# Optimization experiments

Measured on AMD Instinct MI355X. Metric: run time of the kernel, lower is better.

## Reference

```python
import jax, jax.numpy as jnp
import numpy as np

N_USERS = 100000
N_GAMES = 50000
D = 128
E = 1600000


def setup_inputs() -> dict:
    key = jax.random.key(0)
    k1, k2, k3, k4 = jax.random.split(key, 4)
    user_h = jax.random.normal(k1, (N_USERS, D), dtype=jnp.float32)
    game_h = jax.random.normal(k2, (N_GAMES, D), dtype=jnp.float32)
    src_idx = jax.random.randint(k3, (E,), 0, N_USERS, dtype=jnp.int64)
    dst_idx = jax.random.randint(k4, (E,), 0, N_GAMES, dtype=jnp.int64)
    return {"user_h": user_h, "game_h": game_h, "src_idx": src_idx, "dst_idx": dst_idx}


def reference(user_h, game_h, src_idx, dst_idx):
    # DGL fn.u_dot_v: gather src/dst node features along the edge list,
    # then per-edge dot product. Output shape [E, 1] (DGL keeps last dim).
    u = user_h[src_idx]          # [E, D] gather
    v = game_h[dst_idx]          # [E, D] gather
    score = jnp.sum(u * v, axis=-1, keepdims=True)  # [E, 1]
    return score
```

## Files before the change

### kernel.cpp

```cpp
#include <hip/hip_runtime.h>


#define DIM 128
#define NB 64
#define CAP 28160
#define BPB 782
#define N_USERS_C 100000u
#define EPB_A 4096

__global__ void init_cursors(unsigned* __restrict__ cur) {
    int i = threadIdx.x;
    if (i < NB) cur[i * 32] = (unsigned)(i * CAP);
}

__device__ inline unsigned bf16rn(float f) {
    unsigned x = __float_as_uint(f);
    return (x + 0x7FFFu + ((x >> 16) & 1u)) >> 16;
}

__global__ void __launch_bounds__(256) prep_fused(
    const float* __restrict__ user_h, const float* __restrict__ game_h,
    const int* __restrict__ src_idx, const int* __restrict__ dst_idx, int E,
    unsigned* __restrict__ cursors, uint2* __restrict__ records,
    uint4* __restrict__ user_bf, uint4* __restrict__ game_bf,
    int nscat, int nublk, int nu8, int ng8)
{
    __shared__ unsigned hist[NB];
    __shared__ unsigned base_s[NB];
    __shared__ unsigned lcur[NB];
    int bid = blockIdx.x;
    int tid = threadIdx.x;

    if (bid >= nscat) {
        const float* in;
        uint4* outp;
        int i, n8;
        if (bid < nscat + nublk) {
            i = (bid - nscat) * 256 + tid;  n8 = nu8;  in = user_h;  outp = user_bf;
        } else {
            i = (bid - nscat - nublk) * 256 + tid;  n8 = ng8;  in = game_h;  outp = game_bf;
        }
        if (i < n8) {
            const float4* in4 = (const float4*)in;
            float4 a = in4[2 * i];
            float4 b = in4[2 * i + 1];
            uint4 o;
            o.x = bf16rn(a.x) | (bf16rn(a.y) << 16);
            o.y = bf16rn(a.z) | (bf16rn(a.w) << 16);
            o.z = bf16rn(b.x) | (bf16rn(b.y) << 16);
            o.w = bf16rn(b.z) | (bf16rn(b.w) << 16);
            outp[i] = o;
        }
        return;
    }

    long long start = (long long)bid * EPB_A;

    if (tid < NB) hist[tid] = 0u;
    __syncthreads();

    for (int k = 0; k < EPB_A / 256; ++k) {
        long long e = start + k * 256 + tid;
        if (e < E) {
            unsigned s = (unsigned)src_idx[e];
            unsigned b = (s * (unsigned)NB) / N_USERS_C;
            atomicAdd(&hist[b], 1u);
        }
    }
    __syncthreads();

    if (tid < NB) {
        base_s[tid] = atomicAdd(&cursors[tid * 32], hist[tid]);
        lcur[tid] = 0u;
    }
    __syncthreads();

    for (int k = 0; k < EPB_A / 256; ++k) {
        long long e = start + k * 256 + tid;
        if (e < E) {
            unsigned s = (unsigned)src_idx[e];
            unsigned d = (unsigned)dst_idx[e];
            unsigned b = (s * (unsigned)NB) / N_USERS_C;
            unsigned r = atomicAdd(&lcur[b], 1u);
            unsigned pos = base_s[b] + r;
            if (pos < (unsigned)((b + 1) * CAP)) {
                uint2 rec;
                rec.x = s | ((d & 0x7FFFu) << 17);
                rec.y = (d >> 15) | ((unsigned)e << 1);
                records[pos] = rec;
            }
        }
    }
}

__device__ inline float dot8_bf16(uint4 a, uint4 b) {
    float s;
    s  = __uint_as_float(a.x << 16)          * __uint_as_float(b.x << 16);
    s += __uint_as_float(a.x & 0xFFFF0000u)  * __uint_as_float(b.x & 0xFFFF0000u);
    s += __uint_as_float(a.y << 16)          * __uint_as_float(b.y << 16);
    s += __uint_as_float(a.y & 0xFFFF0000u)  * __uint_as_float(b.y & 0xFFFF0000u);
    s += __uint_as_float(a.z << 16)          * __uint_as_float(b.z << 16);
    s += __uint_as_float(a.z & 0xFFFF0000u)  * __uint_as_float(b.z & 0xFFFF0000u);
    s += __uint_as_float(a.w << 16)          * __uint_as_float(b.w << 16);
    s += __uint_as_float(a.w & 0xFFFF0000u)  * __uint_as_float(b.w & 0xFFFF0000u);
    return s;
}

__global__ void __launch_bounds__(256) edge_dot_bucketed_bf16(
    const uint4* __restrict__ user_bf, const uint4* __restrict__ game_bf,
    const unsigned* __restrict__ cursors, const uint2* __restrict__ records,
    float* __restrict__ out)
{
    int bid = blockIdx.x;
    int x = bid & 7;
    int n = bid >> 3;
    int bq = n / BPB;
    int chunk = n - bq * BPB;
    int b = x + 8 * bq;

    int count = (int)(cursors[b * 32] - (unsigned)(b * CAP));
    if (count > CAP) count = CAP;
    const uint2* __restrict__ rec = records + (size_t)b * CAP;

    int g    = threadIdx.x >> 4;
    int lane = threadIdx.x & 15;

    for (int j0 = chunk * 32; j0 < count; j0 += BPB * 32) {
        int j = j0 + 2 * g;
        if (j >= count) continue;
        bool has1 = (j + 1 < count);

        uint2 r0 = rec[j];
        uint2 r1 = has1 ? rec[j + 1] : r0;

        unsigned s0 = r0.x & 0x1FFFFu;
        unsigned d0 = ((r0.x >> 17) & 0x7FFFu) | ((r0.y & 1u) << 15);
        unsigned e0 = r0.y >> 1;
        unsigned s1 = r1.x & 0x1FFFFu;
        unsigned d1 = ((r1.x >> 17) & 0x7FFFu) | ((r1.y & 1u) << 15);
        unsigned e1 = r1.y >> 1;

        uint4 ua = user_bf[(size_t)s0 * 16 + lane];
        uint4 va = game_bf[(size_t)d0 * 16 + lane];
        uint4 ub = user_bf[(size_t)s1 * 16 + lane];
        uint4 vb = game_bf[(size_t)d1 * 16 + lane];

        float sum0 = dot8_bf16(ua, va);
        float sum1 = dot8_bf16(ub, vb);

        sum0 += __shfl_xor(sum0, 1);  sum1 += __shfl_xor(sum1, 1);
        sum0 += __shfl_xor(sum0, 2);  sum1 += __shfl_xor(sum1, 2);
        sum0 += __shfl_xor(sum0, 4);  sum1 += __shfl_xor(sum1, 4);
        sum0 += __shfl_xor(sum0, 8);  sum1 += __shfl_xor(sum1, 8);

        if (lane == 0) {
            out[e0] = sum0;
            if (has1) out[e1] = sum1;
        }
    }
}

__global__ void __launch_bounds__(256) edge_dot_kernel(
    const float* __restrict__ user_h,
    const float* __restrict__ game_h,
    const int* __restrict__ src_idx,
    const int* __restrict__ dst_idx,
    float* __restrict__ out,
    int E)
{
    int tid  = blockIdx.x * blockDim.x + threadIdx.x;
    int g    = tid >> 4;
    int lane = tid & 15;
    long long e0 = (long long)g * 2;
    if (e0 >= E) return;
    bool has1 = (e0 + 1 < E);

    int s0 = src_idx[e0];
    int d0 = dst_idx[e0];
    int s1 = has1 ? src_idx[e0 + 1] : s0;
    int d1 = has1 ? dst_idx[e0 + 1] : d0;

    const float4* __restrict__ u0 = (const float4*)(user_h + (size_t)s0 * DIM);
    const float4* __restrict__ v0 = (const float4*)(game_h + (size_t)d0 * DIM);
    const float4* __restrict__ u1 = (const float4*)(user_h + (size_t)s1 * DIM);
    const float4* __restrict__ v1 = (const float4*)(game_h + (size_t)d1 * DIM);

    float4 ua0 = u0[lane];
    float4 ua1 = u0[lane + 16];
    float4 va0 = v0[lane];
    float4 va1 = v0[lane + 16];
    float4 ub0 = u1[lane];
    float4 ub1 = u1[lane + 16];
    float4 vb0 = v1[lane];
    float4 vb1 = v1[lane + 16];

    float sum0 = ua0.x * va0.x + ua0.y * va0.y + ua0.z * va0.z + ua0.w * va0.w
               + ua1.x * va1.x + ua1.y * va1.y + ua1.z * va1.z + ua1.w * va1.w;
    float sum1 = ub0.x * vb0.x + ub0.y * vb0.y + ub0.z * vb0.z + ub0.w * vb0.w
               + ub1.x * vb1.x + ub1.y * vb1.y + ub1.z * vb1.z + ub1.w * vb1.w;

    sum0 += __shfl_xor(sum0, 1);  sum1 += __shfl_xor(sum1, 1);
    sum0 += __shfl_xor(sum0, 2);  sum1 += __shfl_xor(sum1, 2);
    sum0 += __shfl_xor(sum0, 4);  sum1 += __shfl_xor(sum1, 4);
    sum0 += __shfl_xor(sum0, 8);  sum1 += __shfl_xor(sum1, 8);

    if (lane == 0) {
        out[e0] = sum0;
        if (has1) out[e0 + 1] = sum1;
    }
}

extern "C" void kernel_launch(void* const* d_in, const int* in_sizes, int n_in,
                              void* d_out, int out_size, void* d_ws, size_t ws_size,
                              hipStream_t stream) {
    const float* user_h  = (const float*)d_in[0];
    const float* game_h  = (const float*)d_in[1];
    const int*   src_idx = (const int*)d_in[2];
    const int*   dst_idx = (const int*)d_in[3];
    float*       out     = (float*)d_out;

    int E       = in_sizes[2];
    int n_user  = in_sizes[0];
    int n_game  = in_sizes[1];

    size_t rec_bytes = (size_t)NB * CAP * sizeof(uint2);
    size_t ws_full   = 8192 + rec_bytes + (size_t)n_user * 2 + (size_t)n_game * 2;

    if (ws_size < ws_full || E > (1 << 21)) {
        long long nblocks = ((long long)E + 31) / 32;
        edge_dot_kernel<<<(int)nblocks, 256, 0, stream>>>(
            user_h, game_h, src_idx, dst_idx, out, E);
        return;
    }

    unsigned* cursors = (unsigned*)d_ws;
    uint2*    records = (uint2*)((char*)d_ws + 8192);
    uint4*    user_bf = (uint4*)((char*)d_ws + 8192 + rec_bytes);
    uint4*    game_bf = (uint4*)((char*)user_bf + (size_t)n_user * 2);

    init_cursors<<<1, 64, 0, stream>>>(cursors);

    int nu8 = n_user / 8, ng8 = n_game / 8;
    int nscat = (E + EPB_A - 1) / EPB_A;
    int nublk = (nu8 + 255) / 256;
    int ngblk = (ng8 + 255) / 256;

    prep_fused<<<nscat + nublk + ngblk, 256, 0, stream>>>(
        user_h, game_h, src_idx, dst_idx, E,
        cursors, records, user_bf, game_bf,
        nscat, nublk, nu8, ng8);

    edge_dot_bucketed_bf16<<<NB * BPB, 256, 0, stream>>>(
        user_bf, game_bf, cursors, records, out);
}
```

Measured before the change: 105.7 us.

## Read user features as fp32 directly, convert only game table to bf16

Drops the bf16 conversion of the user table. Because edges are bucketed by source, user rows are read in fp32 straight from the input while only the game table is converted to bf16. This removes a full user-table read and write pass in prep, at the cost of twice the bytes per user-row gather in the dot kernel. The change also replaces the cursor-init kernel with a memset, making cursors zero-based, and keeps the src/dst indices in registers so the scatter pass does not reload them.

```diff
diff --git a/kernel.cpp b/kernel.cpp
--- a/kernel.cpp
+++ b/kernel.cpp
@@ -8,22 +8,17 @@
 #define N_USERS_C 100000u
 #define EPB_A 4096
 
-__global__ void init_cursors(unsigned* __restrict__ cur) {
-    int i = threadIdx.x;
-    if (i < NB) cur[i * 32] = (unsigned)(i * CAP);
-}
-
 __device__ inline unsigned bf16rn(float f) {
     unsigned x = __float_as_uint(f);
     return (x + 0x7FFFu + ((x >> 16) & 1u)) >> 16;
 }
 
 __global__ void __launch_bounds__(256) prep_fused(
-    const float* __restrict__ user_h, const float* __restrict__ game_h,
+    const float* __restrict__ game_h,
     const int* __restrict__ src_idx, const int* __restrict__ dst_idx, int E,
     unsigned* __restrict__ cursors, uint2* __restrict__ records,
-    uint4* __restrict__ user_bf, uint4* __restrict__ game_bf,
-    int nscat, int nublk, int nu8, int ng8)
+    uint4* __restrict__ game_bf,
+    int nscat, int ng8)
 {
     __shared__ unsigned hist[NB];
     __shared__ unsigned base_s[NB];
@@ -32,16 +27,9 @@
     int tid = threadIdx.x;
 
     if (bid >= nscat) {
-        const float* in;
-        uint4* outp;
-        int i, n8;
-        if (bid < nscat + nublk) {
-            i = (bid - nscat) * 256 + tid;  n8 = nu8;  in = user_h;  outp = user_bf;
-        } else {
-            i = (bid - nscat - nublk) * 256 + tid;  n8 = ng8;  in = game_h;  outp = game_bf;
-        }
-        if (i < n8) {
-            const float4* in4 = (const float4*)in;
+        int i = (bid - nscat) * 256 + tid;
+        if (i < ng8) {
+            const float4* in4 = (const float4*)game_h;
             float4 a = in4[2 * i];
             float4 b = in4[2 * i + 1];
             uint4 o;
@@ -49,21 +37,29 @@
             o.y = bf16rn(a.z) | (bf16rn(a.w) << 16);
             o.z = bf16rn(b.x) | (bf16rn(b.y) << 16);
             o.w = bf16rn(b.z) | (bf16rn(b.w) << 16);
-            outp[i] = o;
+            game_bf[i] = o;
         }
         return;
     }
 
     long long start = (long long)bid * EPB_A;
+    unsigned ss[16], dd[16];
+
+    #pragma unroll
+    for (int k = 0; k < 16; ++k) {
+        long long e = start + k * 256 + tid;
+        bool v = (e < E);
+        ss[k] = v ? (unsigned)src_idx[e] : 0xFFFFFFFFu;
+        dd[k] = v ? (unsigned)dst_idx[e] : 0u;
+    }
 
     if (tid < NB) hist[tid] = 0u;
     __syncthreads();
 
-    for (int k = 0; k < EPB_A / 256; ++k) {
-        long long e = start + k * 256 + tid;
-        if (e < E) {
-            unsigned s = (unsigned)src_idx[e];
-            unsigned b = (s * (unsigned)NB) / N_USERS_C;
+    #pragma unroll
+    for (int k = 0; k < 16; ++k) {
+        if (ss[k] != 0xFFFFFFFFu) {
+            unsigned b = (ss[k] * (unsigned)NB) / N_USERS_C;
             atomicAdd(&hist[b], 1u);
         }
     }
@@ -75,39 +71,39 @@
     }
     __syncthreads();
 
-    for (int k = 0; k < EPB_A / 256; ++k) {
-        long long e = start + k * 256 + tid;
-        if (e < E) {
-            unsigned s = (unsigned)src_idx[e];
-            unsigned d = (unsigned)dst_idx[e];
+    #pragma unroll
+    for (int k = 0; k < 16; ++k) {
+        if (ss[k] != 0xFFFFFFFFu) {
+            unsigned s = ss[k], d = dd[k];
             unsigned b = (s * (unsigned)NB) / N_USERS_C;
             unsigned r = atomicAdd(&lcur[b], 1u);
-            unsigned pos = base_s[b] + r;
-            if (pos < (unsigned)((b + 1) * CAP)) {
+            unsigned pr = base_s[b] + r;
+            if (pr < (unsigned)CAP) {
+                long long e = start + k * 256 + tid;
                 uint2 rec;
                 rec.x = s | ((d & 0x7FFFu) << 17);
                 rec.y = (d >> 15) | ((unsigned)e << 1);
-                records[pos] = rec;
+                records[(size_t)b * CAP + pr] = rec;
             }
         }
     }
 }
 
-__device__ inline float dot8_bf16(uint4 a, uint4 b) {
+__device__ inline float dot8_mixed(float4 a0, float4 a1, uint4 b) {
     float s;
-    s  = __uint_as_float(a.x << 16)          * __uint_as_float(b.x << 16);
-    s += __uint_as_float(a.x & 0xFFFF0000u)  * __uint_as_float(b.x & 0xFFFF0000u);
-    s += __uint_as_float(a.y << 16)          * __uint_as_float(b.y << 16);
-    s += __uint_as_float(a.y & 0xFFFF0000u)  * __uint_as_float(b.y & 0xFFFF0000u);
-    s += __uint_as_float(a.z << 16)          * __uint_as_float(b.z << 16);
-    s += __uint_as_float(a.z & 0xFFFF0000u)  * __uint_as_float(b.z & 0xFFFF0000u);
-    s += __uint_as_float(a.w << 16)          * __uint_as_float(b.w << 16);
-    s += __uint_as_float(a.w & 0xFFFF0000u)  * __uint_as_float(b.w & 0xFFFF0000u);
+    s  = a0.x * __uint_as_float(b.x << 16);
+    s += a0.y * __uint_as_float(b.x & 0xFFFF0000u);
+    s += a0.z * __uint_as_float(b.y << 16);
+    s += a0.w * __uint_as_float(b.y & 0xFFFF0000u);
+    s += a1.x * __uint_as_float(b.z << 16);
+    s += a1.y * __uint_as_float(b.z & 0xFFFF0000u);
+    s += a1.z * __uint_as_float(b.w << 16);
+    s += a1.w * __uint_as_float(b.w & 0xFFFF0000u);
     return s;
 }
 
-__global__ void __launch_bounds__(256) edge_dot_bucketed_bf16(
-    const uint4* __restrict__ user_bf, const uint4* __restrict__ game_bf,
+__global__ void __launch_bounds__(256) edge_dot_bucketed_mixed(
+    const float* __restrict__ user_h, const uint4* __restrict__ game_bf,
     const unsigned* __restrict__ cursors, const uint2* __restrict__ records,
     float* __restrict__ out)
 {
@@ -118,7 +114,7 @@
     int chunk = n - bq * BPB;
     int b = x + 8 * bq;
 
-    int count = (int)(cursors[b * 32] - (unsigned)(b * CAP));
+    int count = (int)cursors[b * 32];
     if (count > CAP) count = CAP;
     const uint2* __restrict__ rec = records + (size_t)b * CAP;
 
@@ -140,13 +136,18 @@
         unsigned d1 = ((r1.x >> 17) & 0x7FFFu) | ((r1.y & 1u) << 15);
         unsigned e1 = r1.y >> 1;
 
-        uint4 ua = user_bf[(size_t)s0 * 16 + lane];
-        uint4 va = game_bf[(size_t)d0 * 16 + lane];
-        uint4 ub = user_bf[(size_t)s1 * 16 + lane];
-        uint4 vb = game_bf[(size_t)d1 * 16 + lane];
-
-        float sum0 = dot8_bf16(ua, va);
-        float sum1 = dot8_bf16(ub, vb);
+        const float4* __restrict__ u0 = (const float4*)(user_h + (size_t)s0 * DIM);
+        const float4* __restrict__ u1 = (const float4*)(user_h + (size_t)s1 * DIM);
+
+        float4 ua0 = u0[2 * lane];
+        float4 ua1 = u0[2 * lane + 1];
+        uint4  va  = game_bf[(size_t)d0 * 16 + lane];
+        float4 ub0 = u1[2 * lane];
+        float4 ub1 = u1[2 * lane + 1];
+        uint4  vb  = game_bf[(size_t)d1 * 16 + lane];
+
+        float sum0 = dot8_mixed(ua0, ua1, va);
+        float sum1 = dot8_mixed(ub0, ub1, vb);
 
         sum0 += __shfl_xor(sum0, 1);  sum1 += __shfl_xor(sum1, 1);
         sum0 += __shfl_xor(sum0, 2);  sum1 += __shfl_xor(sum1, 2);
@@ -220,11 +221,10 @@
     float*       out     = (float*)d_out;
 
     int E       = in_sizes[2];
-    int n_user  = in_sizes[0];
     int n_game  = in_sizes[1];
 
     size_t rec_bytes = (size_t)NB * CAP * sizeof(uint2);
-    size_t ws_full   = 8192 + rec_bytes + (size_t)n_user * 2 + (size_t)n_game * 2;
+    size_t ws_full   = 8192 + rec_bytes + (size_t)n_game * 2;
 
     if (ws_size < ws_full || E > (1 << 21)) {
         long long nblocks = ((long long)E + 31) / 32;
@@ -235,21 +235,19 @@
 
     unsigned* cursors = (unsigned*)d_ws;
     uint2*    records = (uint2*)((char*)d_ws + 8192);
-    uint4*    user_bf = (uint4*)((char*)d_ws + 8192 + rec_bytes);
-    uint4*    game_bf = (uint4*)((char*)user_bf + (size_t)n_user * 2);
-
-    init_cursors<<<1, 64, 0, stream>>>(cursors);
-
-    int nu8 = n_user / 8, ng8 = n_game / 8;
+    uint4*    game_bf = (uint4*)((char*)d_ws + 8192 + rec_bytes);
+
+    hipMemsetAsync(cursors, 0, 8192, stream);
+
+    int ng8   = n_game / 8;
     int nscat = (E + EPB_A - 1) / EPB_A;
-    int nublk = (nu8 + 255) / 256;
     int ngblk = (ng8 + 255) / 256;
 
-    prep_fused<<<nscat + nublk + ngblk, 256, 0, stream>>>(
-        user_h, game_h, src_idx, dst_idx, E,
-        cursors, records, user_bf, game_bf,
-        nscat, nublk, nu8, ng8);
-
-    edge_dot_bucketed_bf16<<<NB * BPB, 256, 0, stream>>>(
-        user_bf, game_bf, cursors, records, out);
-}
+    prep_fused<<<nscat + ngblk, 256, 0, stream>>>(
+        game_h, src_idx, dst_idx, E,
+        cursors, records, game_bf,
+        nscat, ng8);
+
+    edge_dot_bucketed_mixed<<<NB * BPB, 256, 0, stream>>>(
+        user_h, game_bf, cursors, records, out);
+}
```

Result: no change. 103.8 us (-1.8%).
